# Kernel optimization log

Hardware: AMD Instinct MI355X
Metric: run time of the kernel (lower is better)

The kernel has to match this reference:

```python
import jax, jax.numpy as jnp
import numpy as np

EPS = 1e-5
THRESH = 0.05
NUM_THINGS = 3
D = 256
EGO_PC_RANGE = np.array([-51.2, -51.2, -5.0, 51.2, 51.2, 3.0], np.float32)


def _inverse_sigmoid(x):
    x = jnp.clip(x, 0.0, 1.0)
    return jnp.log(jnp.maximum(x, EPS) / jnp.maximum(1.0 - x, EPS))


def setup_inputs() -> dict:
    key = jax.random.key(0)
    ks = jax.random.split(key, 16)
    L, B, Qo, Qv = 6, 1, 8192, 8192
    # class logits uniform in [0,1) -> sigmoid >= 0.5 > threshold, so all queries pass (deterministic shapes)
    other_outputs_classes = jax.random.uniform(ks[0], (L, B, Qo, NUM_THINGS), jnp.float32)
    other_outputs_coords = jax.random.uniform(ks[1], (L, B, Qo, 4), jnp.float32)
    other_query = jax.random.normal(ks[2], (B, Qo, D), jnp.float32)
    other_query_pos = jax.random.normal(ks[3], (B, Qo, D), jnp.float32)
    other_reference = jax.random.normal(ks[4], (B, Qo, 4), jnp.float32)
    veh_outputs_classes = jax.random.normal(ks[5], (L, B, Qv, NUM_THINGS), jnp.float32)
    veh_outputs_coords = jax.random.uniform(ks[6], (L, B, Qv, 4), jnp.float32)
    veh_query = jax.random.normal(ks[7], (B, Qv, D), jnp.float32)
    veh_query_pos = jax.random.normal(ks[8], (B, Qv, D), jnp.float32)
    veh_reference = jax.random.normal(ks[9], (B, Qv, 4), jnp.float32)
    # rigid ego->other transform (rotation about z + translation), invertible by construction
    th = 0.3
    rt = np.eye(4, dtype=np.float32)
    rt[0, 0] = np.cos(th); rt[0, 1] = -np.sin(th)
    rt[1, 0] = np.sin(th); rt[1, 1] = np.cos(th)
    rt[0, 3] = 12.0; rt[1, 3] = -5.0; rt[2, 3] = 0.3
    ego2other_rt = jnp.asarray(rt)[None]  # [1,4,4]
    other_agent_pc_range = jnp.asarray(EGO_PC_RANGE)
    xav = float(np.sqrt(2.0 / (D + 9 + D)))
    Wa = jax.random.normal(ks[10], (D + 9, D), jnp.float32) * xav
    ba = jax.random.normal(ks[11], (D,), jnp.float32) * 0.01
    Wp = jax.random.normal(ks[12], (D + 9, D), jnp.float32) * xav
    bp = jax.random.normal(ks[13], (D,), jnp.float32) * 0.01
    return dict(other_outputs_classes=other_outputs_classes, other_outputs_coords=other_outputs_coords,
                other_query=other_query, other_query_pos=other_query_pos, other_reference=other_reference,
                veh_outputs_classes=veh_outputs_classes, veh_outputs_coords=veh_outputs_coords,
                veh_query=veh_query, veh_query_pos=veh_query_pos, veh_reference=veh_reference,
                ego2other_rt=ego2other_rt, other_agent_pc_range=other_agent_pc_range,
                Wa=Wa, ba=ba, Wp=Wp, bp=bp)


def reference(other_outputs_classes, other_outputs_coords, other_query, other_query_pos, other_reference,
              veh_outputs_classes, veh_outputs_coords, veh_query, veh_query_pos, veh_reference,
              ego2other_rt, other_agent_pc_range, Wa, ba, Wp, bp):
    calib = jnp.linalg.inv(ego2other_rt[0].T)  # other -> ego, [4,4]
    # filter_other_lanes (eager: concrete inputs, data-dependent selection like torch.where)
    cls = jax.nn.sigmoid(other_outputs_classes[-1])
    bbox_index = jnp.where(cls.reshape(-1) > THRESH)[0] // NUM_THINGS
    ooc_cls = other_outputs_classes[:, :, bbox_index]      # [L,B,N,3]
    ooc = other_outputs_coords[:, :, bbox_index]           # [L,B,N,4]
    oq = other_query[:, bbox_index]                        # [B,N,D]
    oqp = other_query_pos[:, bbox_index]
    oref = other_reference[:, bbox_index]                  # [B,N,4]
    lo, hi = other_agent_pc_range[:3], other_agent_pc_range[3:]
    elo = jnp.asarray(EGO_PC_RANGE[:3]); ehi = jnp.asarray(EGO_PC_RANGE[3:])
    # --- reference points: inverse_sigmoid space, z logit = 0 ---
    p = jax.nn.sigmoid(jnp.concatenate([oref[..., :2], jnp.zeros_like(oref[..., :1])], -1))
    p = p * (hi - lo) + lo                                 # other lidar coords
    h = jnp.concatenate([p, jnp.ones_like(p[..., :1])], -1)
    p = jnp.einsum('ij,bnj->bni', calib, h)[..., :3]       # ego lidar coords
    p = _inverse_sigmoid((p - elo) / (ehi - elo))
    oref = jnp.concatenate([p[..., :2], oref[..., 2:]], -1)
    # --- bbox centers: already sigmoided, z norm = 0 ---
    b = jnp.concatenate([ooc[..., :2], jnp.zeros_like(ooc[..., :1])], -1)
    b = b * (hi - lo) + lo
    hb = jnp.concatenate([b, jnp.ones_like(b[..., :1])], -1)
    b = jnp.einsum('ij,lbnj->lbni', calib, hb)[..., :3]
    b = (b - elo) / (ehi - elo)
    ooc = jnp.concatenate([b[..., :2], ooc[..., 2:]], -1)
    # --- cross-agent query alignment: concat flattened 3x3 rotation, small Linear ---
    r9 = jnp.broadcast_to(calib[:3, :3].reshape(9), oq.shape[:2] + (9,))
    oq = jnp.concatenate([oq, r9], -1) @ Wa + ba
    oqp = jnp.concatenate([oqp, r9], -1) @ Wp + bp
    return (jnp.concatenate([veh_outputs_classes, ooc_cls], axis=2),
            jnp.concatenate([veh_outputs_coords, ooc], axis=2),
            jnp.concatenate([veh_query, oq], axis=1),
            jnp.concatenate([veh_query_pos, oqp], axis=1),
            jnp.concatenate([veh_reference, oref], axis=1))
```

## Files before the change

kernel.cpp:

```cpp
#include <hip/hip_runtime.h>
#include <stdint.h>

typedef float f32x4 __attribute__((ext_vector_type(4)));
typedef __bf16 bf16x8 __attribute__((ext_vector_type(8)));

namespace {
constexpr int L = 6, Qo = 8192, Qv = 8192, NT = 3, D = 256;
constexpr int ROWS = Qv + 3 * Qo;
constexpr int OUT0 = 0;
constexpr int OUT1 = L * ROWS * NT;
constexpr int OUT2 = OUT1 + L * ROWS * 4;
constexpr int OUT3 = OUT2 + ROWS * D;
constexpr int OUT4 = OUT3 + ROWS * D;
constexpr float ELO0 = -51.2f, ELO1 = -51.2f, EHI0 = 51.2f, EHI1 = 51.2f;
constexpr int NB_GEMM = 512;
constexpr int NB_STREAM = 1536;
constexpr int NB_TOT = NB_GEMM + NB_STREAM;
constexpr int LDSW = 0;
constexpr int LDSA = 8192;
constexpr int LDSBIAS = LDSA + 16384;
constexpr int LDSCAL = LDSBIAS + 128;
constexpr int R_COPY = 2 * Qv * D / 4;
constexpr int R_OUT1 = R_COPY + L * ROWS;
constexpr int R_OUT4 = R_OUT1 + ROWS;
constexpr int R_TOT  = R_OUT4 + L * ROWS * NT / 4;
}

__device__ __forceinline__ float sigmoidf(float x) { return 1.f / (1.f + __expf(-x)); }
__device__ __forceinline__ float invsig(float v) {
    float x = fminf(fmaxf(v, 0.f), 1.f);
    return __logf(fmaxf(x, 1e-5f) / fmaxf(1.f - x, 1e-5f));
}

__device__ void inv4x4_T(const float* __restrict__ rt, float* __restrict__ C) {
    float m[16], inv[16];
    for (int i = 0; i < 4; i++)
        for (int j = 0; j < 4; j++) m[i * 4 + j] = rt[j * 4 + i];
    inv[0]  =  m[5]*m[10]*m[15] - m[5]*m[11]*m[14] - m[9]*m[6]*m[15] + m[9]*m[7]*m[14] + m[13]*m[6]*m[11] - m[13]*m[7]*m[10];
    inv[4]  = -m[4]*m[10]*m[15] + m[4]*m[11]*m[14] + m[8]*m[6]*m[15] - m[8]*m[7]*m[14] - m[12]*m[6]*m[11] + m[12]*m[7]*m[10];
    inv[8]  =  m[4]*m[9]*m[15]  - m[4]*m[11]*m[13] - m[8]*m[5]*m[15] + m[8]*m[7]*m[13] + m[12]*m[5]*m[11] - m[12]*m[7]*m[9];
    inv[12] = -m[4]*m[9]*m[14]  + m[4]*m[10]*m[13] + m[8]*m[5]*m[14] - m[8]*m[6]*m[13] - m[12]*m[5]*m[10] + m[12]*m[6]*m[9];
    inv[1]  = -m[1]*m[10]*m[15] + m[1]*m[11]*m[14] + m[9]*m[2]*m[15] - m[9]*m[3]*m[14] - m[13]*m[2]*m[11] + m[13]*m[3]*m[10];
    inv[5]  =  m[0]*m[10]*m[15] - m[0]*m[11]*m[14] - m[8]*m[2]*m[15] + m[8]*m[3]*m[14] + m[12]*m[2]*m[11] - m[12]*m[3]*m[10];
    inv[9]  = -m[0]*m[9]*m[15]  + m[0]*m[11]*m[13] + m[8]*m[1]*m[15] - m[8]*m[3]*m[13] - m[12]*m[1]*m[11] + m[12]*m[3]*m[9];
    inv[13] =  m[0]*m[9]*m[14]  - m[0]*m[10]*m[13] - m[8]*m[1]*m[14] + m[8]*m[2]*m[13] + m[12]*m[1]*m[10] - m[12]*m[2]*m[9];
    inv[2]  =  m[1]*m[6]*m[15]  - m[1]*m[7]*m[14]  - m[5]*m[2]*m[15] + m[5]*m[3]*m[14] + m[13]*m[2]*m[7]  - m[13]*m[3]*m[6];
    inv[6]  = -m[0]*m[6]*m[15]  + m[0]*m[7]*m[14]  + m[4]*m[2]*m[15] - m[4]*m[3]*m[14] - m[12]*m[2]*m[7]  + m[12]*m[3]*m[6];
    inv[10] =  m[0]*m[5]*m[15]  - m[0]*m[7]*m[13]  - m[4]*m[1]*m[15] + m[4]*m[3]*m[13] + m[12]*m[1]*m[7]  - m[12]*m[3]*m[5];
    inv[14] = -m[0]*m[5]*m[14]  + m[0]*m[6]*m[13]  + m[4]*m[1]*m[14] - m[4]*m[2]*m[13] - m[12]*m[1]*m[6]  + m[12]*m[2]*m[5];
    inv[3]  = -m[1]*m[6]*m[11]  + m[1]*m[7]*m[10]  + m[5]*m[2]*m[11] - m[5]*m[3]*m[10] - m[9]*m[2]*m[7]   + m[9]*m[3]*m[6];
    inv[7]  =  m[0]*m[6]*m[11]  - m[0]*m[7]*m[10]  - m[4]*m[2]*m[11] + m[4]*m[3]*m[10] + m[8]*m[2]*m[7]   - m[8]*m[3]*m[6];
    inv[11] = -m[0]*m[5]*m[11]  + m[0]*m[7]*m[9]   + m[4]*m[1]*m[11] - m[4]*m[3]*m[9]  - m[8]*m[1]*m[7]   + m[8]*m[3]*m[5];
    inv[15] =  m[0]*m[5]*m[10]  - m[0]*m[6]*m[9]   - m[4]*m[1]*m[10] + m[4]*m[2]*m[9]  + m[8]*m[1]*m[6]   - m[8]*m[2]*m[5];
    float det = m[0]*inv[0] + m[1]*inv[4] + m[2]*inv[8] + m[3]*inv[12];
    det = 1.0f / det;
    for (int i = 0; i < 16; i++) C[i] = inv[i] * det;
}

__global__ __launch_bounds__(256, 5) void fused(
    const float* __restrict__ ocls, const float* __restrict__ ocoord,
    const float* __restrict__ oq, const float* __restrict__ oqp,
    const float* __restrict__ oref, const float* __restrict__ vcls,
    const float* __restrict__ vcoord, const float* __restrict__ vq,
    const float* __restrict__ vqp, const float* __restrict__ vref,
    const float* __restrict__ rt, const float* __restrict__ pcr,
    const float* __restrict__ Wa, const float* __restrict__ ba,
    const float* __restrict__ Wp, const float* __restrict__ bp,
    float* __restrict__ out) {
    __shared__ __attribute__((aligned(16))) char lds[24768];
    float* ldsBias  = (float*)&lds[LDSBIAS];
    float* ldsCalib = (float*)&lds[LDSCAL];
    const int b = blockIdx.x;
    const int t = threadIdx.x;

    if (b < NB_GEMM) {
        const int r = b & 7, ny = (b >> 3) & 7, s = b >> 6;
        const int u = s * 8 + r, which = u >> 5, mg = u & 31;
        const float* Asrc = which ? oqp : oq;
        const float* Wsrc = which ? Wp : Wa;
        const float* bv   = which ? bp : ba;
        const size_t obase = which ? (size_t)OUT3 : (size_t)OUT2;
        const int n0 = ny * 32;
        if (t == 0) inv4x4_T(rt, ldsCalib);
        __syncthreads();
        if (t < 32) {
            float sum = bv[n0 + t];
            #pragma unroll
            for (int m2 = 0; m2 < 9; m2++)
                sum += ldsCalib[(m2 / 3) * 4 + (m2 % 3)] * Wsrc[(size_t)(D + m2) * D + n0 + t];
            ldsBias[t] = sum;
        }
        const int lane = t & 63, wave = t >> 6, lrow = lane & 15, grp = lane >> 4;
        const int arow = wave * 16 + lrow;
        const int aswz = (arow & 7) << 4;
        f32x4 acc[4][2] = {};
        #pragma unroll
        for (int half = 0; half < 2; ++half) {
            #pragma unroll
            for (int mi = 0; mi < 4; ++mi) {
                __syncthreads();
                if (mi == 0) {
                    int n4 = (t & 7) * 4;
                    int kb0 = t >> 3;
                    #pragma unroll
                    for (int pass = 0; pass < 4; ++pass) {
                        int kl = pass * 32 + kb0;
                        f32x4 v = *(const f32x4*)&Wsrc[(size_t)(half * 128 + kl) * D + n0 + n4];
                        #pragma unroll
                        for (int i = 0; i < 4; ++i) {
                            int n = n4 + i;
                            *(__bf16*)&lds[LDSW + n * 256 + ((2 * kl) ^ ((n & 7) << 4))] =
                                (__bf16)v[i];
                        }
                    }
                }
                const float* Abase = Asrc + (size_t)(mg * 4 + mi) * 64 * D + half * 128;
                #pragma unroll
                for (int i = 0; i < 4; ++i) {
                    int flat = i * 256 + t;
                    int row = flat >> 4;
                    int cu8 = flat & 15;
                    const float* src = Abase + (size_t)row * D + cu8 * 8;
                    f32x4 a0 = *(const f32x4*)src;
                    f32x4 a1 = *(const f32x4*)(src + 4);
                    bf16x8 w = {(__bf16)a0.x, (__bf16)a0.y, (__bf16)a0.z, (__bf16)a0.w,
                                (__bf16)a1.x, (__bf16)a1.y, (__bf16)a1.z, (__bf16)a1.w};
                    *(bf16x8*)&lds[LDSA + row * 256 + ((cu8 * 16) ^ ((row & 7) << 4))] = w;
                }
                __syncthreads();
                #pragma unroll
                for (int ks = 0; ks < 4; ++ks) {
                    int kb = ks * 64 + grp * 16;
                    bf16x8 af = *(const bf16x8*)&lds[LDSA + arow * 256 + (kb ^ aswz)];
                    #pragma unroll
                    for (int nt = 0; nt < 2; ++nt) {
                        int c = nt * 16 + lrow;
                        bf16x8 w = *(const bf16x8*)&lds[LDSW + c * 256 + (kb ^ ((c & 7) << 4))];
                        acc[mi][nt] =
                            __builtin_amdgcn_mfma_f32_16x16x32_bf16(w, af, acc[mi][nt], 0, 0, 0);
                    }
                }
            }
        }
        #pragma unroll
        for (int mi = 0; mi < 4; ++mi) {
            const int am = (mg * 4 + mi) * 64 + arow;
            size_t rbase = obase + (size_t)(Qv + 3 * am) * D + n0;
            #pragma unroll
            for (int nt = 0; nt < 2; ++nt) {
                f32x4 bz = *(const f32x4*)&ldsBias[nt * 16 + grp * 4];
                f32x4 v = acc[mi][nt] + bz;
                float* p = out + rbase + nt * 16 + grp * 4;
                *(f32x4*)p = v;
                *(f32x4*)(p + D) = v;
                *(f32x4*)(p + 2 * D) = v;
            }
        }
        return;
    }

    if (t == 0) inv4x4_T(rt, ldsCalib);
    __syncthreads();
    const float c00 = ldsCalib[0], c01 = ldsCalib[1], c02 = ldsCalib[2], c03 = ldsCalib[3];
    const float c10 = ldsCalib[4], c11 = ldsCalib[5], c12 = ldsCalib[6], c13 = ldsCalib[7];
    const float lo0 = pcr[0], lo1 = pcr[1], lo2 = pcr[2];
    const float hi0 = pcr[3], hi1 = pcr[4], hi2 = pcr[5];
    const int stride = NB_STREAM * 256;
    for (int c = (b - NB_GEMM) * 256 + t; c < R_TOT; c += stride) {
        if (c < R_COPY) {
            const int HALF = Qv * D / 4;
            const float* src = (c < HALF) ? vq : vqp;
            size_t ob = (c < HALF) ? (size_t)OUT2 : (size_t)OUT3;
            int jj = (c < HALF) ? c : c - HALF;
            *(f32x4*)&out[ob + (size_t)jj * 4] = *(const f32x4*)&src[(size_t)jj * 4];
        } else if (c < R_OUT1) {
            int tid = c - R_COPY;
            unsigned l = (unsigned)tid >> 15, rr = (unsigned)tid & 32767u;
            f32x4 o;
            if (rr < (unsigned)Qv) {
                o = *(const f32x4*)&vcoord[((size_t)l * Qv + rr) * 4];
            } else {
                unsigned q = (rr - Qv) / 3u;
                f32x4 s = *(const f32x4*)&ocoord[((size_t)l * Qo + q) * 4];
                float bx = s.x * (hi0 - lo0) + lo0;
                float by = s.y * (hi1 - lo1) + lo1;
                float bz = lo2;
                float px = c00 * bx + c01 * by + c02 * bz + c03;
                float py = c10 * bx + c11 * by + c12 * bz + c13;
                o.x = (px - ELO0) / (EHI0 - ELO0);
                o.y = (py - ELO1) / (EHI1 - ELO1);
                o.z = s.z; o.w = s.w;
            }
            *(f32x4*)&out[OUT1 + (size_t)tid * 4] = o;
        } else if (c < R_OUT4) {
            unsigned rr = (unsigned)(c - R_OUT1);
            f32x4 o;
            if (rr < (unsigned)Qv) {
                o = *(const f32x4*)&vref[(size_t)rr * 4];
            } else {
                unsigned q = (rr - Qv) / 3u;
                f32x4 s = *(const f32x4*)&oref[(size_t)q * 4];
                float bx = sigmoidf(s.x) * (hi0 - lo0) + lo0;
                float by = sigmoidf(s.y) * (hi1 - lo1) + lo1;
                float bz = 0.5f * (hi2 - lo2) + lo2;
                float px = c00 * bx + c01 * by + c02 * bz + c03;
                float py = c10 * bx + c11 * by + c12 * bz + c13;
                o.x = invsig((px - ELO0) / (EHI0 - ELO0));
                o.y = invsig((py - ELO1) / (EHI1 - ELO1));
                o.z = s.z; o.w = s.w;
            }
            *(f32x4*)&out[OUT4 + (size_t)rr * 4] = o;
        } else {
            int e0 = (c - R_OUT4) * 4;
            f32x4 o;
            #pragma unroll
            for (int i = 0; i < 4; ++i) {
                unsigned e = (unsigned)(e0 + i);
                unsigned l = e / (unsigned)(ROWS * NT);
                unsigned rem = e - l * (ROWS * NT);
                unsigned rr = rem / 3u;
                float v;
                if (rr < (unsigned)Qv) v = vcls[l * (Qv * NT) + rem];
                else {
                    unsigned cc = rem - rr * 3u;
                    unsigned q = (rr - Qv) / 3u;
                    v = ocls[l * (Qo * NT) + q * 3u + cc];
                }
                o[i] = v;
            }
            *(f32x4*)&out[OUT0 + (size_t)e0] = o;
        }
    }
}

extern "C" void kernel_launch(void* const* d_in, const int* in_sizes, int n_in,
                              void* d_out, int out_size, void* d_ws, size_t ws_size,
                              hipStream_t stream) {
    const float* ocls   = (const float*)d_in[0];
    const float* ocoord = (const float*)d_in[1];
    const float* oq     = (const float*)d_in[2];
    const float* oqp    = (const float*)d_in[3];
    const float* oref   = (const float*)d_in[4];
    const float* vcls   = (const float*)d_in[5];
    const float* vcoord = (const float*)d_in[6];
    const float* vq     = (const float*)d_in[7];
    const float* vqp    = (const float*)d_in[8];
    const float* vref   = (const float*)d_in[9];
    const float* rt     = (const float*)d_in[10];
    const float* pcr    = (const float*)d_in[11];
    const float* Wa     = (const float*)d_in[12];
    const float* ba     = (const float*)d_in[13];
    const float* Wp     = (const float*)d_in[14];
    const float* bp     = (const float*)d_in[15];
    float* out = (float*)d_out;

    hipLaunchKernelGGL(fused, dim3(NB_TOT), dim3(256), 0, stream,
                       ocls, ocoord, oq, oqp, oref, vcls, vcoord, vq, vqp, vref,
                       rt, pcr, Wa, ba, Wp, bp, out);
}
```

Baseline: 31.20 us.

## Shrink GEMM tile to 128 rows, preload full-K weights, compute calib per-thread

Each GEMM block now covers 128 rows of A instead of 256, which doubles the GEMM block count. Each block loads the full 256-deep weight slice into LDS once, and the M/K loop order is swapped so only two accumulators stay live. Every thread now computes the 4x4 inverse and the folded bias in registers, which removes the LDS calib/bias staging and its barriers in both the GEMM and streaming paths. The intent is more parallelism and lower register pressure, at the cost of 32KB LDS per block (lower occupancy), redundant per-thread matrix inversion, and re-reading weights in twice as many blocks.

```diff
diff --git a/kernel.cpp b/kernel.cpp
--- a/kernel.cpp
+++ b/kernel.cpp
@@ -13,13 +13,11 @@
 constexpr int OUT3 = OUT2 + ROWS * D;
 constexpr int OUT4 = OUT3 + ROWS * D;
 constexpr float ELO0 = -51.2f, ELO1 = -51.2f, EHI0 = 51.2f, EHI1 = 51.2f;
-constexpr int NB_GEMM = 512;
+constexpr int NB_GEMM = 1024;
 constexpr int NB_STREAM = 1536;
 constexpr int NB_TOT = NB_GEMM + NB_STREAM;
 constexpr int LDSW = 0;
-constexpr int LDSA = 8192;
-constexpr int LDSBIAS = LDSA + 16384;
-constexpr int LDSCAL = LDSBIAS + 128;
+constexpr int LDSA = 16384;
 constexpr int R_COPY = 2 * Qv * D / 4;
 constexpr int R_OUT1 = R_COPY + L * ROWS;
 constexpr int R_OUT4 = R_OUT1 + ROWS;
@@ -32,9 +30,11 @@
     return __logf(fmaxf(x, 1e-5f) / fmaxf(1.f - x, 1e-5f));
 }
 
-__device__ void inv4x4_T(const float* __restrict__ rt, float* __restrict__ C) {
+__device__ __forceinline__ void inv4x4_T(const float* __restrict__ rt, float* C) {
     float m[16], inv[16];
+    #pragma unroll
     for (int i = 0; i < 4; i++)
+        #pragma unroll
         for (int j = 0; j < 4; j++) m[i * 4 + j] = rt[j * 4 + i];
     inv[0]  =  m[5]*m[10]*m[15] - m[5]*m[11]*m[14] - m[9]*m[6]*m[15] + m[9]*m[7]*m[14] + m[13]*m[6]*m[11] - m[13]*m[7]*m[10];
     inv[4]  = -m[4]*m[10]*m[15] + m[4]*m[11]*m[14] + m[8]*m[6]*m[15] - m[8]*m[7]*m[14] - m[12]*m[6]*m[11] + m[12]*m[7]*m[10];
@@ -54,6 +54,7 @@
     inv[15] =  m[0]*m[5]*m[10]  - m[0]*m[6]*m[9]   - m[4]*m[1]*m[10] + m[4]*m[2]*m[9]  + m[8]*m[1]*m[6]   - m[8]*m[2]*m[5];
     float det = m[0]*inv[0] + m[1]*inv[4] + m[2]*inv[8] + m[3]*inv[12];
     det = 1.0f / det;
+    #pragma unroll
     for (int i = 0; i < 16; i++) C[i] = inv[i] * det;
 }
 
@@ -67,54 +68,58 @@
     const float* __restrict__ Wa, const float* __restrict__ ba,
     const float* __restrict__ Wp, const float* __restrict__ bp,
     float* __restrict__ out) {
-    __shared__ __attribute__((aligned(16))) char lds[24768];
-    float* ldsBias  = (float*)&lds[LDSBIAS];
-    float* ldsCalib = (float*)&lds[LDSCAL];
+    __shared__ __attribute__((aligned(16))) char lds[32768];
     const int b = blockIdx.x;
     const int t = threadIdx.x;
 
     if (b < NB_GEMM) {
-        const int r = b & 7, ny = (b >> 3) & 7, s = b >> 6;
-        const int u = s * 8 + r, which = u >> 5, mg = u & 31;
+        const int ny = b >> 7, rem = b & 127, which = rem >> 6, mg = rem & 63;
         const float* Asrc = which ? oqp : oq;
         const float* Wsrc = which ? Wp : Wa;
         const float* bv   = which ? bp : ba;
         const size_t obase = which ? (size_t)OUT3 : (size_t)OUT2;
         const int n0 = ny * 32;
-        if (t == 0) inv4x4_T(rt, ldsCalib);
-        __syncthreads();
-        if (t < 32) {
-            float sum = bv[n0 + t];
-            #pragma unroll
-            for (int m2 = 0; m2 < 9; m2++)
-                sum += ldsCalib[(m2 / 3) * 4 + (m2 % 3)] * Wsrc[(size_t)(D + m2) * D + n0 + t];
-            ldsBias[t] = sum;
-        }
         const int lane = t & 63, wave = t >> 6, lrow = lane & 15, grp = lane >> 4;
+
+        f32x4 bz[2];
+        {
+            float C[16];
+            inv4x4_T(rt, C);
+            #pragma unroll
+            for (int nt = 0; nt < 2; ++nt) {
+                int c = n0 + nt * 16 + grp * 4;
+                f32x4 s = *(const f32x4*)&bv[c];
+                #pragma unroll
+                for (int m2 = 0; m2 < 9; ++m2) {
+                    float r = C[(m2 / 3) * 4 + (m2 % 3)];
+                    f32x4 w = *(const f32x4*)&Wsrc[(size_t)(D + m2) * D + c];
+                    s += w * r;
+                }
+                bz[nt] = s;
+            }
+        }
+        {
+            int kloc = t >> 3, n4 = (t & 7) * 4;
+            #pragma unroll
+            for (int pass = 0; pass < 8; ++pass) {
+                int k = pass * 32 + kloc;
+                f32x4 v = *(const f32x4*)&Wsrc[(size_t)k * D + n0 + n4];
+                #pragma unroll
+                for (int i = 0; i < 4; ++i) {
+                    int n = n4 + i;
+                    *(__bf16*)&lds[LDSW + n * 512 + ((2 * k) ^ ((n & 7) << 4))] = (__bf16)v[i];
+                }
+            }
+        }
         const int arow = wave * 16 + lrow;
         const int aswz = (arow & 7) << 4;
-        f32x4 acc[4][2] = {};
         #pragma unroll
-        for (int half = 0; half < 2; ++half) {
-            #pragma unroll
-            for (int mi = 0; mi < 4; ++mi) {
+        for (int mi = 0; mi < 2; ++mi) {
+            f32x4 acc[2] = {f32x4{0, 0, 0, 0}, f32x4{0, 0, 0, 0}};
+            #pragma unroll
+            for (int half = 0; half < 2; ++half) {
                 __syncthreads();
-                if (mi == 0) {
-                    int n4 = (t & 7) * 4;
-                    int kb0 = t >> 3;
-                    #pragma unroll
-                    for (int pass = 0; pass < 4; ++pass) {
-                        int kl = pass * 32 + kb0;
-                        f32x4 v = *(const f32x4*)&Wsrc[(size_t)(half * 128 + kl) * D + n0 + n4];
-                        #pragma unroll
-                        for (int i = 0; i < 4; ++i) {
-                            int n = n4 + i;
-                            *(__bf16*)&lds[LDSW + n * 256 + ((2 * kl) ^ ((n & 7) << 4))] =
-                                (__bf16)v[i];
-                        }
-                    }
-                }
-                const float* Abase = Asrc + (size_t)(mg * 4 + mi) * 64 * D + half * 128;
+                const float* Abase = Asrc + (size_t)(mg * 128 + mi * 64) * D + half * 128;
                 #pragma unroll
                 for (int i = 0; i < 4; ++i) {
                     int flat = i * 256 + t;
@@ -130,26 +135,23 @@
                 __syncthreads();
                 #pragma unroll
                 for (int ks = 0; ks < 4; ++ks) {
-                    int kb = ks * 64 + grp * 16;
-                    bf16x8 af = *(const bf16x8*)&lds[LDSA + arow * 256 + (kb ^ aswz)];
+                    int kbA = ks * 64 + grp * 16;
+                    bf16x8 af = *(const bf16x8*)&lds[LDSA + arow * 256 + (kbA ^ aswz)];
+                    int kbW = half * 256 + kbA;
                     #pragma unroll
                     for (int nt = 0; nt < 2; ++nt) {
                         int c = nt * 16 + lrow;
-                        bf16x8 w = *(const bf16x8*)&lds[LDSW + c * 256 + (kb ^ ((c & 7) << 4))];
-                        acc[mi][nt] =
-                            __builtin_amdgcn_mfma_f32_16x16x32_bf16(w, af, acc[mi][nt], 0, 0, 0);
+                        bf16x8 w =
+                            *(const bf16x8*)&lds[LDSW + c * 512 + (kbW ^ ((c & 7) << 4))];
+                        acc[nt] = __builtin_amdgcn_mfma_f32_16x16x32_bf16(w, af, acc[nt], 0, 0, 0);
                     }
                 }
             }
-        }
-        #pragma unroll
-        for (int mi = 0; mi < 4; ++mi) {
-            const int am = (mg * 4 + mi) * 64 + arow;
+            const int am = mg * 128 + mi * 64 + arow;
             size_t rbase = obase + (size_t)(Qv + 3 * am) * D + n0;
             #pragma unroll
             for (int nt = 0; nt < 2; ++nt) {
-                f32x4 bz = *(const f32x4*)&ldsBias[nt * 16 + grp * 4];
-                f32x4 v = acc[mi][nt] + bz;
+                f32x4 v = acc[nt] + bz[nt];
                 float* p = out + rbase + nt * 16 + grp * 4;
                 *(f32x4*)p = v;
                 *(f32x4*)(p + D) = v;
@@ -159,10 +161,10 @@
         return;
     }
 
-    if (t == 0) inv4x4_T(rt, ldsCalib);
-    __syncthreads();
-    const float c00 = ldsCalib[0], c01 = ldsCalib[1], c02 = ldsCalib[2], c03 = ldsCalib[3];
-    const float c10 = ldsCalib[4], c11 = ldsCalib[5], c12 = ldsCalib[6], c13 = ldsCalib[7];
+    float C[16];
+    inv4x4_T(rt, C);
+    const float c00 = C[0], c01 = C[1], c02 = C[2], c03 = C[3];
+    const float c10 = C[4], c11 = C[5], c12 = C[6], c13 = C[7];
     const float lo0 = pcr[0], lo1 = pcr[1], lo2 = pcr[2];
     const float hi0 = pcr[3], hi1 = pcr[4], hi2 = pcr[5];
     const int stride = NB_STREAM * 256;
```

New measurement: 34.22 us. 1.1x slower.
